# Kernel tuning notes

Measured on AMD Instinct MI355X. Metric: run time of the kernel, lower is better.

## Reference

```python
import jax, jax.numpy as jnp
import numpy as np

EMB_DIM = 300
TEMPERATURE = 0.01
REWEIGHT = True
N = 8192
NUM_GROUPS = 100


def setup_inputs() -> dict:
    key = jax.random.key(0)
    ks = jax.random.split(key, 6)
    s = 1.0 / np.sqrt(EMB_DIM)
    x = jax.random.normal(ks[0], (N, EMB_DIM), dtype=jnp.float32)
    W1 = jax.random.normal(ks[1], (EMB_DIM, EMB_DIM), dtype=jnp.float32) * s
    b1 = jnp.zeros((EMB_DIM,), dtype=jnp.float32)
    W2 = jax.random.normal(ks[2], (EMB_DIM, EMB_DIM), dtype=jnp.float32) * s
    b2 = jnp.zeros((EMB_DIM,), dtype=jnp.float32)
    # labels in [1, 100]: all > 0 so the group_y>0 filter keeps every row
    labels = jax.random.randint(ks[3], (N,), 1, NUM_GROUPS + 1, dtype=jnp.int32)
    return {"x": x, "W1": W1, "b1": b1, "W2": W2, "b2": b2, "labels": labels}


def reference(x, W1, b1, W2, b2, labels):
    # projector: Linear -> ReLU -> Linear
    h = jax.nn.relu(x @ W1 + b1) @ W2 + b2
    # L2 normalize rows
    f = h / jnp.linalg.norm(h, axis=1, keepdims=True)
    # pairwise similarity / temperature, row-max subtracted (detached)
    logits = (f @ f.T) / TEMPERATURE                      # [N, N]
    logits = logits - jax.lax.stop_gradient(jnp.max(logits, axis=1, keepdims=True))

    lab = labels[:, None]
    mask = (lab == lab.T).astype(logits.dtype)            # same-group mask
    logits_mask = 1.0 - jnp.eye(mask.shape[0], dtype=logits.dtype)  # drop diagonal
    mask = mask * logits_mask

    # rows with at least one positive (torch filters these; we weight instead)
    pos_count = jnp.sum(mask, axis=1)                     # [N]
    valid = pos_count > 0

    if REWEIGHT:
        pos_m = logits_mask * mask
        neg_m = logits_mask * (1.0 - mask)
        pos_sum = jnp.sum(pos_m, axis=1, keepdims=True)
        neg_sum = jnp.sum(neg_m, axis=1, keepdims=True)
        log_pos = jnp.where(pos_sum > 0, jnp.log(jnp.maximum(pos_sum, 1.0)), 0.0)
        log_neg = jnp.where(neg_sum > 0, jnp.log(jnp.maximum(neg_sum, 1.0)), 0.0)
        logits = (logits - log_pos) * pos_m + (logits - log_neg) * neg_m

    exp_logits = jnp.exp(logits) * logits_mask
    log_prob = logits - jnp.log(jnp.sum(exp_logits, axis=1, keepdims=True))
    mean_log_prob_pos = jnp.sum(mask * log_prob, axis=1) / jnp.where(valid, pos_count, 1.0)
    validf = valid.astype(logits.dtype)
    loss = -TEMPERATURE * jnp.sum(mean_log_prob_pos * validf) / jnp.sum(validf)
    return loss
```

## Files before the change

kernel.cpp:

```cpp
#include <hip/hip_runtime.h>
#include <hip/hip_bf16.h>


#define N_ROWS 8192
#define D_PAD 320
#define NG 100
#define TEMP 0.01f
#define NSPLIT 32
#define JCHUNK (N_ROWS / NSPLIT)
#define LOG2E100 144.2695041f

typedef short short8v __attribute__((ext_vector_type(8)));
typedef float float4v __attribute__((ext_vector_type(4)));

__device__ __forceinline__ short f2bf(float f) {
  union { __hip_bfloat16 h; short s; } u;
  u.h = __float2bfloat16(f);
  return u.s;
}

__global__ __launch_bounds__(256) void setup_kernel(
    const float* __restrict__ W1, const float* __restrict__ W2,
    const int* __restrict__ labels,
    __hip_bfloat16* __restrict__ w1t, __hip_bfloat16* __restrict__ w2t,
    int* __restrict__ counts32)
{
  __shared__ float T[64][65];
  __shared__ int hc[NG + 1];
  int b = blockIdx.x, tid = threadIdx.x;
  if (b < 50) {
    int isW2 = b >= 25;
    int t5 = isW2 ? b - 25 : b;
    int k0 = (t5 / 5) * 64, n0 = (t5 % 5) * 64;
    const float* W = isW2 ? W2 : W1;
    __hip_bfloat16* dst = isW2 ? w2t : w1t;
#pragma unroll
    for (int t = 0; t < 16; ++t) {
      int e = tid + t * 256;
      int r = e >> 6, c = e & 63;
      T[r][c] = (k0 + r < 300 && n0 + c < 300)
                  ? W[(size_t)(k0 + r) * 300 + (n0 + c)] : 0.0f;
    }
    __syncthreads();
#pragma unroll
    for (int t = 0; t < 16; ++t) {
      int e = tid + t * 256;
      int nn = e >> 6, kk = e & 63;
      dst[(size_t)(n0 + nn) * D_PAD + (k0 + kk)] = __float2bfloat16(T[kk][nn]);
    }
  } else {
    int h = b - 50;
    if (tid <= NG) hc[tid] = 0;
    __syncthreads();
    atomicAdd(&hc[labels[h * 256 + tid]], 1);
    __syncthreads();
    if (tid <= NG) counts32[h * (NG + 1) + tid] = hc[tid];
  }
}

__global__ __launch_bounds__(256) void mlp_fused_kernel(
    const float* __restrict__ x, const __hip_bfloat16* __restrict__ w1t,
    const __hip_bfloat16* __restrict__ w2t, const float* __restrict__ b1,
    const float* __restrict__ b2, __hip_bfloat16* __restrict__ fb)
{
  __shared__ __align__(16) short H1[32 * D_PAD];
  __shared__ float ssq_s[32];
  const short* W1s = (const short*)w1t;
  const short* W2s = (const short*)w2t;
  int tid = threadIdx.x;
  int lane = tid & 63, wave = tid >> 6;
  int strip = wave >> 1, p = wave & 1;
  int g = lane >> 4, lc = lane & 15, sw = lc & 7;
  int i0 = blockIdx.x * 32;

  if (tid < 32) ssq_s[tid] = 0.f;

  short8v afr[10];
  {
    const float* xp = x + (size_t)(i0 + strip * 16 + lc) * 300;
#pragma unroll
    for (int kk = 0; kk < 10; ++kk) {
      int k0 = kk * 32 + g * 8;
      short8v v;
      if (k0 + 8 <= 300) {
        float4 a = *(const float4*)(xp + k0);
        float4 c = *(const float4*)(xp + k0 + 4);
        v[0] = f2bf(a.x); v[1] = f2bf(a.y); v[2] = f2bf(a.z); v[3] = f2bf(a.w);
        v[4] = f2bf(c.x); v[5] = f2bf(c.y); v[6] = f2bf(c.z); v[7] = f2bf(c.w);
      } else if (k0 < 300) {
        float4 a = *(const float4*)(xp + k0);
        v[0] = f2bf(a.x); v[1] = f2bf(a.y); v[2] = f2bf(a.z); v[3] = f2bf(a.w);
        v[4] = 0; v[5] = 0; v[6] = 0; v[7] = 0;
      } else {
        v = short8v{0, 0, 0, 0, 0, 0, 0, 0};
      }
      afr[kk] = v;
    }
  }

  for (int nt = 0; nt < 10; ++nt) {
    int n = (p * 10 + nt) * 16 + lc;
    float4v acc = {0.f, 0.f, 0.f, 0.f};
    const short* wp = W1s + (size_t)n * D_PAD + g * 8;
#pragma unroll
    for (int kk = 0; kk < 10; ++kk) {
      short8v bf = *(const short8v*)(wp + kk * 32);
      acc = __builtin_amdgcn_mfma_f32_16x16x32_bf16(afr[kk], bf, acc, 0, 0, 0);
    }
    float bv = (n < 300) ? b1[n] : 0.0f;
    int q = n >> 3;
#pragma unroll
    for (int r = 0; r < 4; ++r) {
      int row = strip * 16 + g * 4 + r;
      H1[row * D_PAD + ((q ^ (row & 7)) << 3) + (n & 7)] =
          f2bf(fmaxf(acc[r] + bv, 0.0f));
    }
  }
  __syncthreads();

  short8v hfr[10];
  {
    const short* rp = H1 + (strip * 16 + lc) * D_PAD;
#pragma unroll
    for (int kk = 0; kk < 10; ++kk)
      hfr[kk] = *(const short8v*)(rp + (((g + 4 * kk) ^ sw) << 3));
  }

  float4v h2a[10];
  for (int nt = 0; nt < 10; ++nt) {
    int n = (p * 10 + nt) * 16 + lc;
    float4v acc = {0.f, 0.f, 0.f, 0.f};
    const short* wp = W2s + (size_t)n * D_PAD + g * 8;
#pragma unroll
    for (int kk = 0; kk < 10; ++kk) {
      short8v bf = *(const short8v*)(wp + kk * 32);
      acc = __builtin_amdgcn_mfma_f32_16x16x32_bf16(hfr[kk], bf, acc, 0, 0, 0);
    }
    float bv = (n < 300) ? b2[n] : 0.0f;
#pragma unroll
    for (int r = 0; r < 4; ++r) acc[r] += bv;
    h2a[nt] = acc;
  }

  float ss[4] = {0.f, 0.f, 0.f, 0.f};
#pragma unroll
  for (int nt = 0; nt < 10; ++nt)
#pragma unroll
    for (int r = 0; r < 4; ++r) ss[r] = fmaf(h2a[nt][r], h2a[nt][r], ss[r]);
  for (int m = 1; m < 16; m <<= 1)
#pragma unroll
    for (int r = 0; r < 4; ++r) ss[r] += __shfl_xor(ss[r], m, 64);
  if (lc == 0)
#pragma unroll
    for (int r = 0; r < 4; ++r) atomicAdd(&ssq_s[strip * 16 + g * 4 + r], ss[r]);
  __syncthreads();
  float inv[4];
#pragma unroll
  for (int r = 0; r < 4; ++r) inv[r] = rsqrtf(ssq_s[strip * 16 + g * 4 + r]);
#pragma unroll
  for (int nt = 0; nt < 10; ++nt) {
    int n = (p * 10 + nt) * 16 + lc;
#pragma unroll
    for (int r = 0; r < 4; ++r) {
      int row = i0 + strip * 16 + g * 4 + r;
      fb[(size_t)row * D_PAD + n] = __float2bfloat16(h2a[nt][r] * inv[r]);
    }
  }
}

__global__ __launch_bounds__(256, 3) void pg_kernel(
    const __hip_bfloat16* __restrict__ Fb, const int* __restrict__ labels,
    float* __restrict__ partE, float* __restrict__ sPar, float* __restrict__ sAar)
{
  __shared__ __align__(16) short Bs[64 * D_PAD];
  __shared__ int memb[256];
  __shared__ int cnt;
  const short* Fs = (const short*)Fb;
  int tid = threadIdx.x;
  int lane = tid & 63, wave = tid >> 6;
  int g = lane >> 4, lc = lane & 15, sw = lc & 7;
  int b = blockIdx.x;

  if (b < 2048) {
    int bi = b >> 5, split = b & 31;
    int i0 = bi * 128;
    int jstart = split * JCHUNK;

    short8v afr[2][10];
    for (int s = 0; s < 2; ++s) {
      const short* ap = Fs + (size_t)(i0 + s * 64 + wave * 16 + lc) * D_PAD + g * 8;
#pragma unroll
      for (int kk = 0; kk < 10; ++kk) afr[s][kk] = *(const short8v*)(ap + kk * 32);
    }
    float sE[2][4] = {};

    for (int jt = 0; jt < JCHUNK / 64; ++jt) {
      int jb = jstart + jt * 64;
      __syncthreads();
      {
        const int4* src = (const int4*)Fs;
        int4* dst = (int4*)Bs;
#pragma unroll
        for (int t = 0; t < 10; ++t) {
          int e = tid + t * 256;
          int r = e / 40, q = e - r * 40;
          dst[r * 40 + (q ^ (r & 7))] = src[(size_t)(jb + r) * 40 + q];
        }
      }
      __syncthreads();
      for (int js = 0; js < 4; ++js) {
        float4v acc0 = {0.f, 0.f, 0.f, 0.f}, acc1 = {0.f, 0.f, 0.f, 0.f};
        const short* rowp = Bs + (js * 16 + lc) * D_PAD;
#pragma unroll
        for (int kk = 0; kk < 10; ++kk) {
          short8v bf = *(const short8v*)(rowp + (((g + 4 * kk) ^ sw) << 3));
          acc0 = __builtin_amdgcn_mfma_f32_16x16x32_bf16(afr[0][kk], bf, acc0, 0, 0, 0);
          acc1 = __builtin_amdgcn_mfma_f32_16x16x32_bf16(afr[1][kk], bf, acc1, 0, 0, 0);
        }
#pragma unroll
        for (int s = 0; s < 2; ++s) {
          float4v acc = s ? acc1 : acc0;
          bool dt = (jb == i0 + s * 64) && (js == wave);
#pragma unroll
          for (int r = 0; r < 4; ++r) {
            float e = exp2f(fmaf(acc[r], LOG2E100, -LOG2E100));
            if (dt && lc == g * 4 + r) e = 0.0f;
            sE[s][r] += e;
          }
        }
      }
    }
    for (int m = 1; m < 16; m <<= 1)
#pragma unroll
      for (int s = 0; s < 2; ++s)
#pragma unroll
        for (int r = 0; r < 4; ++r) sE[s][r] += __shfl_xor(sE[s][r], m, 64);
    if (lc == 0)
      for (int s = 0; s < 2; ++s)
        for (int r = 0; r < 4; ++r)
          partE[split * N_ROWS + i0 + s * 64 + wave * 16 + g * 4 + r] = sE[s][r];
  } else {
    int grp = b - 2048 + 1;
    if (tid == 0) cnt = 0;
    __syncthreads();
    for (int i = tid; i < N_ROWS; i += 256)
      if (labels[i] == grp) { int pp = atomicAdd(&cnt, 1); if (pp < 256) memb[pp] = i; }
    __syncthreads();
    int c = cnt > 256 ? 256 : cnt;
    int nt = (c + 63) >> 6;
    for (int it = 0; it < nt; ++it) {
      short8v afr[10];
      {
        int islot = it * 64 + wave * 16 + lc;
        int arow = memb[islot < c ? islot : 0];
        const short* ap = Fs + (size_t)arow * D_PAD + g * 8;
#pragma unroll
        for (int kk = 0; kk < 10; ++kk) afr[kk] = *(const short8v*)(ap + kk * 32);
      }
      int iglobr[4]; bool ivalid[4];
      for (int r = 0; r < 4; ++r) {
        int islot = it * 64 + wave * 16 + g * 4 + r;
        ivalid[r] = islot < c;
        iglobr[r] = memb[islot < c ? islot : 0];
      }
      float sp[4] = {}, sa[4] = {};
      for (int jt = 0; jt < nt; ++jt) {
        __syncthreads();
        {
          const int4* src = (const int4*)Fs;
          int4* dst = (int4*)Bs;
#pragma unroll
          for (int t = 0; t < 10; ++t) {
            int e = tid + t * 256;
            int r = e / 40, q = e - r * 40;
            int jslot = jt * 64 + r;
            int grow = memb[jslot < c ? jslot : 0];
            dst[r * 40 + (q ^ (r & 7))] = src[(size_t)grow * 40 + q];
          }
        }
        __syncthreads();
        for (int js = 0; js < 4; ++js) {
          float4v acc = {0.f, 0.f, 0.f, 0.f};
          const short* rowp = Bs + (js * 16 + lc) * D_PAD;
#pragma unroll
          for (int kk = 0; kk < 10; ++kk) {
            short8v bf = *(const short8v*)(rowp + (((g + 4 * kk) ^ sw) << 3));
            acc = __builtin_amdgcn_mfma_f32_16x16x32_bf16(afr[kk], bf, acc, 0, 0, 0);
          }
          int jslot = jt * 64 + js * 16 + lc;
          bool jv = jslot < c;
          int jglob = memb[jslot < c ? jslot : 0];
#pragma unroll
          for (int r = 0; r < 4; ++r) {
            float a = acc[r];
            float e = exp2f(fmaf(a, LOG2E100, -LOG2E100));
            bool ok = jv && ivalid[r] && (jglob != iglobr[r]);
            sp[r] += ok ? e : 0.f;
            sa[r] += ok ? a : 0.f;
          }
        }
      }
      for (int m = 1; m < 16; m <<= 1)
        for (int r = 0; r < 4; ++r) {
          sp[r] += __shfl_xor(sp[r], m, 64);
          sa[r] += __shfl_xor(sa[r], m, 64);
        }
      if (lc == 0)
        for (int r = 0; r < 4; ++r)
          if (ivalid[r]) { sPar[iglobr[r]] = sp[r]; sAar[iglobr[r]] = sa[r]; }
    }
  }
}

__global__ __launch_bounds__(1024) void final_kernel(
    const float* __restrict__ partE, const float* __restrict__ sPar,
    const float* __restrict__ sAar, const int* __restrict__ counts32,
    const int* __restrict__ labels, float* __restrict__ out)
{
  __shared__ int cnt_s[NG + 1];
  __shared__ float rm[1024], rv[1024];
  int tid = threadIdx.x;
  if (tid <= NG) {
    int c = 0;
    for (int s = 0; s < 32; ++s) c += counts32[s * (NG + 1) + tid];
    cnt_s[tid] = c;
  }
  __syncthreads();
  float sumM = 0.f, sumV = 0.f;
  for (int i = tid; i < N_ROWS; i += 1024) {
    float sE = 0.f;
    for (int s = 0; s < NSPLIT; ++s) sE += partE[s * N_ROWS + i];
    int pc = cnt_s[labels[i]] - 1;
    if (pc > 0) {
      float P = sPar[i], A = sAar[i];
      float Q = sE - P;
      float pcf = (float)pc, ncf = (float)(N_ROWS - 1 - pc);
      float Z = P / pcf + Q / ncf;
      sumM += 100.0f * A / pcf - 100.0f - logf(pcf) - logf(Z);
      sumV += 1.f;
    }
  }
  rm[tid] = sumM; rv[tid] = sumV;
  __syncthreads();
  for (int s = 512; s > 0; s >>= 1) {
    if (tid < s) { rm[tid] += rm[tid + s]; rv[tid] += rv[tid + s]; }
    __syncthreads();
  }
  if (tid == 0) out[0] = (rv[0] > 0.f) ? (-TEMP * rm[0] / rv[0]) : 0.f;
}

extern "C" void kernel_launch(void* const* d_in, const int* in_sizes, int n_in,
                              void* d_out, int out_size, void* d_ws, size_t ws_size,
                              hipStream_t stream)
{
  const float* x  = (const float*)d_in[0];
  const float* W1 = (const float*)d_in[1];
  const float* b1 = (const float*)d_in[2];
  const float* W2 = (const float*)d_in[3];
  const float* b2 = (const float*)d_in[4];
  const int* labels = (const int*)d_in[5];

  char* ws = (char*)d_ws;
  __hip_bfloat16* fb   = (__hip_bfloat16*)(ws);
  __hip_bfloat16* w1t  = (__hip_bfloat16*)(ws + 5242880);
  __hip_bfloat16* w2t  = (__hip_bfloat16*)(ws + 5447680);
  int*         counts32 = (int*)(ws + 5652480);
  float*        partE  = (float*)(ws + 5665536);
  float*        sPar   = (float*)(ws + 6714112);
  float*        sAar   = (float*)(ws + 6746880);

  setup_kernel<<<82, 256, 0, stream>>>(W1, W2, labels, w1t, w2t, counts32);
  mlp_fused_kernel<<<256, 256, 0, stream>>>(x, w1t, w2t, b1, b2, fb);
  pg_kernel<<<2048 + NG, 256, 0, stream>>>(fb, labels, partE, sPar, sAar);
  final_kernel<<<1, 1024, 0, stream>>>(partE, sPar, sAar, counts32, labels, (float*)d_out);
}
```

Baseline: 193.7 us.

## Rebalance MLP, pg and final kernels across more blocks and launches

The MLP kernel now handles 16 rows per block, with each wave covering 5 output tiles, doubling its grid to 512 blocks, and gets a launch bound of 2 blocks per CU. The pair-gram kernel puts the group blocks first and splits its dense blocks over two launches via base offsets, with its occupancy hint lowered from 3 to 2. The single-block final reduction becomes a 32-block partial reduction followed by a one-wave combine. The aim is better CU utilization in the small kernels and a shorter serial tail, at the cost of two extra launches.

Measured after the change: 204.0 us. +5.3%, slower.

```diff
diff --git a/kernel.cpp b/kernel.cpp
--- a/kernel.cpp
+++ b/kernel.cpp
@@ -58,26 +58,25 @@
   }
 }
 
-__global__ __launch_bounds__(256) void mlp_fused_kernel(
+__global__ __launch_bounds__(256, 2) void mlp_fused_kernel(
     const float* __restrict__ x, const __hip_bfloat16* __restrict__ w1t,
     const __hip_bfloat16* __restrict__ w2t, const float* __restrict__ b1,
     const float* __restrict__ b2, __hip_bfloat16* __restrict__ fb)
 {
-  __shared__ __align__(16) short H1[32 * D_PAD];
-  __shared__ float ssq_s[32];
+  __shared__ __align__(16) short H1[16 * D_PAD];
+  __shared__ float ssq_s[16];
   const short* W1s = (const short*)w1t;
   const short* W2s = (const short*)w2t;
   int tid = threadIdx.x;
-  int lane = tid & 63, wave = tid >> 6;
-  int strip = wave >> 1, p = wave & 1;
+  int lane = tid & 63, p = tid >> 6;
   int g = lane >> 4, lc = lane & 15, sw = lc & 7;
-  int i0 = blockIdx.x * 32;
-
-  if (tid < 32) ssq_s[tid] = 0.f;
+  int i0 = blockIdx.x * 16;
+
+  if (tid < 16) ssq_s[tid] = 0.f;
 
   short8v afr[10];
   {
-    const float* xp = x + (size_t)(i0 + strip * 16 + lc) * 300;
+    const float* xp = x + (size_t)(i0 + lc) * 300;
 #pragma unroll
     for (int kk = 0; kk < 10; ++kk) {
       int k0 = kk * 32 + g * 8;
@@ -98,8 +97,8 @@
     }
   }
 
-  for (int nt = 0; nt < 10; ++nt) {
-    int n = (p * 10 + nt) * 16 + lc;
+  for (int nt = 0; nt < 5; ++nt) {
+    int n = (p * 5 + nt) * 16 + lc;
     float4v acc = {0.f, 0.f, 0.f, 0.f};
     const short* wp = W1s + (size_t)n * D_PAD + g * 8;
 #pragma unroll
@@ -111,7 +110,7 @@
     int q = n >> 3;
 #pragma unroll
     for (int r = 0; r < 4; ++r) {
-      int row = strip * 16 + g * 4 + r;
+      int row = g * 4 + r;
       H1[row * D_PAD + ((q ^ (row & 7)) << 3) + (n & 7)] =
           f2bf(fmaxf(acc[r] + bv, 0.0f));
     }
@@ -120,15 +119,15 @@
 
   short8v hfr[10];
   {
-    const short* rp = H1 + (strip * 16 + lc) * D_PAD;
+    const short* rp = H1 + lc * D_PAD;
 #pragma unroll
     for (int kk = 0; kk < 10; ++kk)
       hfr[kk] = *(const short8v*)(rp + (((g + 4 * kk) ^ sw) << 3));
   }
 
-  float4v h2a[10];
-  for (int nt = 0; nt < 10; ++nt) {
-    int n = (p * 10 + nt) * 16 + lc;
+  float4v h2a[5];
+  for (int nt = 0; nt < 5; ++nt) {
+    int n = (p * 5 + nt) * 16 + lc;
     float4v acc = {0.f, 0.f, 0.f, 0.f};
     const short* wp = W2s + (size_t)n * D_PAD + g * 8;
 #pragma unroll
@@ -144,7 +143,7 @@
 
   float ss[4] = {0.f, 0.f, 0.f, 0.f};
 #pragma unroll
-  for (int nt = 0; nt < 10; ++nt)
+  for (int nt = 0; nt < 5; ++nt)
 #pragma unroll
     for (int r = 0; r < 4; ++r) ss[r] = fmaf(h2a[nt][r], h2a[nt][r], ss[r]);
   for (int m = 1; m < 16; m <<= 1)
@@ -152,25 +151,26 @@
     for (int r = 0; r < 4; ++r) ss[r] += __shfl_xor(ss[r], m, 64);
   if (lc == 0)
 #pragma unroll
-    for (int r = 0; r < 4; ++r) atomicAdd(&ssq_s[strip * 16 + g * 4 + r], ss[r]);
+    for (int r = 0; r < 4; ++r) atomicAdd(&ssq_s[g * 4 + r], ss[r]);
   __syncthreads();
   float inv[4];
 #pragma unroll
-  for (int r = 0; r < 4; ++r) inv[r] = rsqrtf(ssq_s[strip * 16 + g * 4 + r]);
-#pragma unroll
-  for (int nt = 0; nt < 10; ++nt) {
-    int n = (p * 10 + nt) * 16 + lc;
+  for (int r = 0; r < 4; ++r) inv[r] = rsqrtf(ssq_s[g * 4 + r]);
+#pragma unroll
+  for (int nt = 0; nt < 5; ++nt) {
+    int n = (p * 5 + nt) * 16 + lc;
 #pragma unroll
     for (int r = 0; r < 4; ++r) {
-      int row = i0 + strip * 16 + g * 4 + r;
+      int row = i0 + g * 4 + r;
       fb[(size_t)row * D_PAD + n] = __float2bfloat16(h2a[nt][r] * inv[r]);
     }
   }
 }
 
-__global__ __launch_bounds__(256, 3) void pg_kernel(
+__global__ __launch_bounds__(256, 2) void pg_kernel(
     const __hip_bfloat16* __restrict__ Fb, const int* __restrict__ labels,
-    float* __restrict__ partE, float* __restrict__ sPar, float* __restrict__ sAar)
+    float* __restrict__ partE, float* __restrict__ sPar, float* __restrict__ sAar,
+    int groupCount, int denseBase)
 {
   __shared__ __align__(16) short Bs[64 * D_PAD];
   __shared__ int memb[256];
@@ -181,8 +181,9 @@
   int g = lane >> 4, lc = lane & 15, sw = lc & 7;
   int b = blockIdx.x;
 
-  if (b < 2048) {
-    int bi = b >> 5, split = b & 31;
+  if (b >= groupCount) {
+    int d = b - groupCount + denseBase;
+    int bi = d >> 5, split = d & 31;
     int i0 = bi * 128;
     int jstart = split * JCHUNK;
 
@@ -240,7 +241,7 @@
         for (int r = 0; r < 4; ++r)
           partE[split * N_ROWS + i0 + s * 64 + wave * 16 + g * 4 + r] = sE[s][r];
   } else {
-    int grp = b - 2048 + 1;
+    int grp = b + 1;
     if (tid == 0) cnt = 0;
     __syncthreads();
     for (int i = tid; i < N_ROWS; i += 256)
@@ -312,41 +313,49 @@
   }
 }
 
-__global__ __launch_bounds__(1024) void final_kernel(
+__global__ __launch_bounds__(256) void final_a_kernel(
     const float* __restrict__ partE, const float* __restrict__ sPar,
     const float* __restrict__ sAar, const int* __restrict__ counts32,
-    const int* __restrict__ labels, float* __restrict__ out)
+    const int* __restrict__ labels, float* __restrict__ blk)
 {
   __shared__ int cnt_s[NG + 1];
-  __shared__ float rm[1024], rv[1024];
+  __shared__ float rm[256], rv[256];
   int tid = threadIdx.x;
+  int i = blockIdx.x * 256 + tid;
   if (tid <= NG) {
     int c = 0;
     for (int s = 0; s < 32; ++s) c += counts32[s * (NG + 1) + tid];
     cnt_s[tid] = c;
   }
+  float sE = 0.f;
+  for (int s = 0; s < NSPLIT; ++s) sE += partE[s * N_ROWS + i];
   __syncthreads();
-  float sumM = 0.f, sumV = 0.f;
-  for (int i = tid; i < N_ROWS; i += 1024) {
-    float sE = 0.f;
-    for (int s = 0; s < NSPLIT; ++s) sE += partE[s * N_ROWS + i];
-    int pc = cnt_s[labels[i]] - 1;
-    if (pc > 0) {
-      float P = sPar[i], A = sAar[i];
-      float Q = sE - P;
-      float pcf = (float)pc, ncf = (float)(N_ROWS - 1 - pc);
-      float Z = P / pcf + Q / ncf;
-      sumM += 100.0f * A / pcf - 100.0f - logf(pcf) - logf(Z);
-      sumV += 1.f;
-    }
-  }
-  rm[tid] = sumM; rv[tid] = sumV;
+  float M = 0.f, V = 0.f;
+  int pc = cnt_s[labels[i]] - 1;
+  if (pc > 0) {
+    float P = sPar[i], A = sAar[i];
+    float Q = sE - P;
+    float pcf = (float)pc, ncf = (float)(N_ROWS - 1 - pc);
+    float Z = P / pcf + Q / ncf;
+    M = 100.0f * A / pcf - 100.0f - logf(pcf) - logf(Z);
+    V = 1.f;
+  }
+  rm[tid] = M; rv[tid] = V;
   __syncthreads();
-  for (int s = 512; s > 0; s >>= 1) {
-    if (tid < s) { rm[tid] += rm[tid + s]; rv[tid] += rv[tid + s]; }
-    __syncthreads();
-  }
-  if (tid == 0) out[0] = (rv[0] > 0.f) ? (-TEMP * rm[0] / rv[0]) : 0.f;
+  for (int s2 = 128; s2 > 0; s2 >>= 1) {
+    if (tid < s2) { rm[tid] += rm[tid + s2]; rv[tid] += rv[tid + s2]; }
+    __syncthreads();
+  }
+  if (tid == 0) { blk[blockIdx.x] = rm[0]; blk[32 + blockIdx.x] = rv[0]; }
+}
+
+__global__ void final_b_kernel(const float* __restrict__ blk, float* __restrict__ out)
+{
+  int lane = threadIdx.x;
+  float m = (lane < 32) ? blk[lane] : 0.f;
+  float v = (lane < 32) ? blk[32 + lane] : 0.f;
+  for (int s = 1; s < 32; s <<= 1) { m += __shfl_xor(m, s, 64); v += __shfl_xor(v, s, 64); }
+  if (lane == 0) out[0] = (v > 0.f) ? (-TEMP * m / v) : 0.f;
 }
 
 extern "C" void kernel_launch(void* const* d_in, const int* in_sizes, int n_in,
@@ -361,16 +370,19 @@
   const int* labels = (const int*)d_in[5];
 
   char* ws = (char*)d_ws;
-  __hip_bfloat16* fb   = (__hip_bfloat16*)(ws);
-  __hip_bfloat16* w1t  = (__hip_bfloat16*)(ws + 5242880);
-  __hip_bfloat16* w2t  = (__hip_bfloat16*)(ws + 5447680);
+  __hip_bfloat16* fb    = (__hip_bfloat16*)(ws);
+  __hip_bfloat16* w1t   = (__hip_bfloat16*)(ws + 5242880);
+  __hip_bfloat16* w2t   = (__hip_bfloat16*)(ws + 5447680);
   int*         counts32 = (int*)(ws + 5652480);
-  float*        partE  = (float*)(ws + 5665536);
-  float*        sPar   = (float*)(ws + 6714112);
-  float*        sAar   = (float*)(ws + 6746880);
+  float*        partE   = (float*)(ws + 5665536);
+  float*        sPar    = (float*)(ws + 6714112);
+  float*        sAar    = (float*)(ws + 6746880);
+  float*        blk     = (float*)(ws + 6779648);
 
   setup_kernel<<<82, 256, 0, stream>>>(W1, W2, labels, w1t, w2t, counts32);
-  mlp_fused_kernel<<<256, 256, 0, stream>>>(x, w1t, w2t, b1, b2, fb);
-  pg_kernel<<<2048 + NG, 256, 0, stream>>>(fb, labels, partE, sPar, sAar);
-  final_kernel<<<1, 1024, 0, stream>>>(partE, sPar, sAar, counts32, labels, (float*)d_out);
-}
+  mlp_fused_kernel<<<512, 256, 0, stream>>>(x, w1t, w2t, b1, b2, fb);
+  pg_kernel<<<NG + 1024, 256, 0, stream>>>(fb, labels, partE, sPar, sAar, NG, 0);
+  pg_kernel<<<1024, 256, 0, stream>>>(fb, labels, partE, sPar, sAar, 0, 1024);
+  final_a_kernel<<<32, 256, 0, stream>>>(partE, sPar, sAar, counts32, labels, blk);
+  final_b_kernel<<<1, 64, 0, stream>>>(blk, (float*)d_out);
+}
```
